# Kernel optimization log

Measured on AMD Instinct MI355X. Metric: run time of the kernel, lower is better.

The kernel has to match this reference:

```python
import jax, jax.numpy as jnp
import numpy as np

N = 50000      # n_nodes
E = 800000     # n_edges (before self loops)
DIN = 128      # in_channels
H = 4          # heads
C = 32         # out_channels per head  (H*C == DIN -> residual is Identity)
EPS = 1e-5
NEG_SLOPE = 0.2


def layer_norm(x, g, b):
    m = jnp.mean(x, axis=-1, keepdims=True)
    v = jnp.mean((x - m) ** 2, axis=-1, keepdims=True)
    return (x - m) * jax.lax.rsqrt(v + EPS) * g + b


def setup_inputs() -> dict:
    key = jax.random.key(0)
    ks = jax.random.split(key, 14)
    s = 1.0 / np.sqrt(DIN)
    return {
        "x": jax.random.normal(ks[0], (N, DIN), dtype=jnp.float32),
        "edge_index": jax.random.randint(ks[1], (2, E), 0, N, dtype=jnp.int64),
        "ln1_g": jnp.ones((DIN,), jnp.float32),
        "ln1_b": jnp.zeros((DIN,), jnp.float32),
        "W": jax.random.normal(ks[2], (DIN, H * C), jnp.float32) * s,
        "att_src": jax.random.normal(ks[3], (H, C), jnp.float32) * (1.0 / np.sqrt(C)),
        "att_dst": jax.random.normal(ks[4], (H, C), jnp.float32) * (1.0 / np.sqrt(C)),
        "gat_b": jnp.zeros((H * C,), jnp.float32),
        "ln2_g": jnp.ones((H * C,), jnp.float32),
        "ln2_b": jnp.zeros((H * C,), jnp.float32),
        "w1": jax.random.normal(ks[5], (H * C, 2 * H * C), jnp.float32) * (1.0 / np.sqrt(H * C)),
        "b1": jnp.zeros((2 * H * C,), jnp.float32),
        "w2": jax.random.normal(ks[6], (2 * H * C, H * C), jnp.float32) * (1.0 / np.sqrt(2 * H * C)),
        "b2": jnp.zeros((H * C,), jnp.float32),
    }


def gat_conv(h, src, dst, W, att_src, att_dst, gat_b, n):
    # linear projection per head: (n, H, C)
    xh = (h @ W).reshape(n, H, C)
    # per-node attention logits: (n, H)
    a_src = jnp.einsum("nhc,hc->nh", xh, att_src)
    a_dst = jnp.einsum("nhc,hc->nh", xh, att_dst)
    # edge scores + segment softmax over destination nodes
    alpha = jax.nn.leaky_relu(a_src[src] + a_dst[dst], NEG_SLOPE)  # (e, H)
    amax = jax.ops.segment_max(alpha, dst, num_segments=n)
    alpha = jnp.exp(alpha - amax[dst])
    denom = jax.ops.segment_sum(alpha, dst, num_segments=n)
    alpha = alpha / denom[dst]
    # weighted aggregation of source features
    msg = xh[src] * alpha[:, :, None]                                # (e, H, C)
    out = jax.ops.segment_sum(msg, dst, num_segments=n)              # (n, H, C)
    return out.reshape(n, H * C) + gat_b


def reference(x, edge_index, ln1_g, ln1_b, W, att_src, att_dst, gat_b,
              ln2_g, ln2_b, w1, b1, w2, b2):
    n = x.shape[0]
    # add self loops (PyG GATConv default add_self_loops=True)
    loops = jnp.arange(n, dtype=edge_index.dtype)
    src = jnp.concatenate([edge_index[0], loops])
    dst = jnp.concatenate([edge_index[1], loops])

    h = layer_norm(x, ln1_g, ln1_b)
    h = gat_conv(h, src, dst, W, att_src, att_dst, gat_b, n)
    h = h + x  # residual is Identity since in_channels == heads*out_channels
    hn = layer_norm(h, ln2_g, ln2_b)
    ffn = jax.nn.gelu(hn @ w1 + b1, approximate=False) @ w2 + b2
    return h + ffn
```

## Files before the change

### kernel.cpp

```cpp
#include <hip/hip_runtime.h>

#define DIN 128
#define HEADS 4
#define CPH 32
#define NEG_SLOPE 0.2f
#define LN_EPS 1e-5f
#define NPB 16
#define CS 4096
#define CE 512

typedef short bf16x8 __attribute__((ext_vector_type(8)));
typedef float f32x4 __attribute__((ext_vector_type(4)));
typedef float f32x2 __attribute__((ext_vector_type(2)));

__device__ __forceinline__ float wave_allsum(float v) {
#pragma unroll
    for (int off = 32; off > 0; off >>= 1) v += __shfl_down(v, off, 64);
    return __shfl(v, 0, 64);
}

__device__ __forceinline__ unsigned short f2bf(float f) {
    unsigned int b = __float_as_uint(f);
    b += 0x7FFFu + ((b >> 16) & 1u);
    return (unsigned short)(b >> 16);
}
__device__ __forceinline__ float bf2f(unsigned short u) {
    return __uint_as_float(((unsigned int)u) << 16);
}

#define ABST 136
#define HST  264
#define SRST 132

__global__ __launch_bounds__(256) void k_hist_pack(
    const int* __restrict__ ei, unsigned int* __restrict__ cnt, int E, int N, int Nper, int HB,
    const float* __restrict__ w1, const float* __restrict__ w2, const float* __restrict__ W,
    unsigned short* __restrict__ wp1, unsigned short* __restrict__ wp2,
    unsigned short* __restrict__ wpW)
{
    int bid = blockIdx.x;
    if (bid < HB) {
        int xcd = bid & 7, chunk = bid >> 3;
        int lo = xcd * Nper, hi = min(lo + Nper, N);
        int Et = E + N;
        int base = chunk * CS + threadIdx.x;
#pragma unroll
        for (int i = 0; i < CS / 256; ++i) {
            int e = base + i * 256;
            if (e >= Et) break;
            int d = (e < E) ? ei[E + e] : (e - E);
            if (d >= lo && d < hi) atomicAdd(&cnt[d], 1u);
        }
    } else {
        int idx = (bid - HB) * 256 + threadIdx.x;
        if (idx < 32768) {
            int j = idx & 7, lane = (idx >> 3) & 63, tk = idx >> 9;
            int ks = tk & 3, tile = tk >> 2;
            int k = ks * 32 + ((lane >> 4) << 3) + j;
            int n = tile * 16 + (lane & 15);
            wp1[idx] = f2bf(w1[k * 256 + n]);
        } else if (idx < 65536) {
            int i2 = idx - 32768;
            int j = i2 & 7, lane = (i2 >> 3) & 63, tk = i2 >> 9;
            int ks = tk & 7, tile = tk >> 3;
            int k = ks * 32 + ((lane >> 4) << 3) + j;
            int n = tile * 16 + (lane & 15);
            wp2[i2] = f2bf(w2[k * 128 + n]);
        } else {
            int i3 = idx - 65536;
            int j = i3 & 7, lane = (i3 >> 3) & 63, tk = i3 >> 9;
            int ks = tk & 3, tile = tk >> 2;
            int k = ks * 32 + ((lane >> 4) << 3) + j;
            int n = tile * 16 + (lane & 15);
            wpW[i3] = f2bf(W[k * 128 + n]);
        }
    }
}

__global__ __launch_bounds__(256) void k_partsum(
    const unsigned int* __restrict__ cnt, unsigned int* __restrict__ bsum, int N)
{
    __shared__ unsigned int sm[4];
    int t = threadIdx.x;
    int i = blockIdx.x * 256 + t;
    unsigned int v = (i < N) ? cnt[i] : 0u;
#pragma unroll
    for (int off = 32; off > 0; off >>= 1) v += (unsigned int)__shfl_down((int)v, off, 64);
    if ((t & 63) == 0) sm[t >> 6] = v;
    __syncthreads();
    if (t == 0) bsum[blockIdx.x] = sm[0] + sm[1] + sm[2] + sm[3];
}

__global__ __launch_bounds__(256) void k_scanb(
    const unsigned int* __restrict__ bsum, unsigned int* __restrict__ boff,
    unsigned int* __restrict__ row, int nb2, int N, int Et)
{
    __shared__ unsigned int sm[256];
    int t = threadIdx.x;
    unsigned int v = (t < nb2) ? bsum[t] : 0u;
    sm[t] = v;
    __syncthreads();
#pragma unroll
    for (int off = 1; off < 256; off <<= 1) {
        unsigned int a = (t >= off) ? sm[t - off] : 0u;
        __syncthreads();
        sm[t] += a;
        __syncthreads();
    }
    if (t < nb2) boff[t] = sm[t] - v;
    if (t == 0) row[N] = (unsigned int)Et;
}

__global__ __launch_bounds__(256) void k_scanw(
    const unsigned int* __restrict__ cnt, const unsigned int* __restrict__ boff,
    unsigned int* __restrict__ row, unsigned int* __restrict__ pos, int N)
{
    __shared__ unsigned int sm[256];
    int t = threadIdx.x;
    int i = blockIdx.x * 256 + t;
    unsigned int v = (i < N) ? cnt[i] : 0u;
    sm[t] = v;
    __syncthreads();
#pragma unroll
    for (int off = 1; off < 256; off <<= 1) {
        unsigned int a = (t >= off) ? sm[t - off] : 0u;
        __syncthreads();
        sm[t] += a;
        __syncthreads();
    }
    if (i < N) {
        unsigned int o = boff[blockIdx.x] + sm[t] - v;
        row[i] = o;
        pos[i] = o;
    }
}

__global__ __launch_bounds__(256) void k_scatter_proj(
    const int* __restrict__ ei, unsigned int* __restrict__ pos,
    int* __restrict__ srcs, int E, int N, int Nper, int SB,
    const float* __restrict__ x,
    const float* __restrict__ g1, const float* __restrict__ b1,
    const unsigned short* __restrict__ wpW,
    const float* __restrict__ att_src, const float* __restrict__ att_dst,
    unsigned short* __restrict__ xhb, float* __restrict__ a_src, float* __restrict__ a_dst)
{
    __shared__ __align__(16) unsigned short A_bf[NPB * ABST];
    __shared__ __align__(16) unsigned short sxh[NPB * ABST];
    int bid = blockIdx.x;
    int t = threadIdx.x;

    if (bid < SB) {
        int xcd = bid & 7, chunk = bid >> 3;
        int lo = xcd * Nper, hi = min(lo + Nper, N);
        int Et = E + N;
        int base = chunk * CS + t;
#pragma unroll
        for (int i = 0; i < CS / 256; ++i) {
            int e = base + i * 256;
            if (e >= Et) break;
            int d = (e < E) ? ei[E + e] : (e - E);
            if (d >= lo && d < hi) {
                int s = (e < E) ? ei[e] : d;
                unsigned int p = atomicAdd(&pos[d], 1u);
                srcs[p] = s;
            }
        }
        return;
    }

    int w = t >> 6, lane = t & 63;
    int quad = lane >> 4, l15 = lane & 15;
    int nbase = (bid - SB) * NPB;

#pragma unroll
    for (int i = 0; i < 4; ++i) {
        int nn = w * 4 + i;
        int n = nbase + nn;
        float x0 = 0.f, x1 = 0.f;
        if (n < N) { x0 = x[n * DIN + lane]; x1 = x[n * DIN + 64 + lane]; }
        float mean = wave_allsum(x0 + x1) * (1.0f / DIN);
        float d0 = x0 - mean, d1 = x1 - mean;
        float var = wave_allsum(d0 * d0 + d1 * d1) * (1.0f / DIN);
        float rstd = rsqrtf(var + LN_EPS);
        A_bf[nn * ABST + lane]      = f2bf(d0 * rstd * g1[lane]      + b1[lane]);
        A_bf[nn * ABST + 64 + lane] = f2bf(d1 * rstd * g1[64 + lane] + b1[64 + lane]);
    }
    __syncthreads();

    {
        int arow = l15 * ABST;
        bf16x8 afrag[4];
#pragma unroll
        for (int ks = 0; ks < 4; ++ks)
            afrag[ks] = *(const bf16x8*)&A_bf[arow + ks * 32 + quad * 8];
#pragma unroll
        for (int nt = 0; nt < 2; ++nt) {
            int tile = w * 2 + nt;
            f32x4 acc = {0.f, 0.f, 0.f, 0.f};
#pragma unroll
            for (int ks = 0; ks < 4; ++ks) {
                bf16x8 bfrag = *(const bf16x8*)&wpW[(((tile * 4 + ks) * 64 + lane) << 3)];
                acc = __builtin_amdgcn_mfma_f32_16x16x32_bf16(afrag[ks], bfrag, acc, 0, 0, 0);
            }
            int col = tile * 16 + l15;
#pragma unroll
            for (int reg = 0; reg < 4; ++reg)
                sxh[(quad * 4 + reg) * ABST + col] = f2bf(acc[reg]);
        }
    }
    __syncthreads();

    {
        int node = t >> 4, off = (t & 15) * 8;
        int n = nbase + node;
        if (n < N)
            *(uint4*)&xhb[(size_t)n * DIN + off] = *(const uint4*)&sxh[node * ABST + off];
    }

    {
        int node = w * 4 + (lane >> 4);
        int h = (lane >> 2) & 3, sub = lane & 3;
        float s1 = 0.f, s2 = 0.f;
#pragma unroll
        for (int i = 0; i < 8; ++i) {
            int c = h * CPH + sub * 8 + i;
            float v = bf2f(sxh[node * ABST + c]);
            s1 += v * att_src[c];
            s2 += v * att_dst[c];
        }
        s1 += __shfl_down(s1, 1, 64); s2 += __shfl_down(s2, 1, 64);
        s1 += __shfl_down(s1, 2, 64); s2 += __shfl_down(s2, 2, 64);
        int n = nbase + node;
        if (sub == 0 && n < N) {
            a_src[n * HEADS + h] = s1;
            a_dst[n * HEADS + h] = s2;
        }
    }
}

__global__ __launch_bounds__(256, 6) void k_agg_final(
    const unsigned int* __restrict__ row, const int* __restrict__ srcs,
    const float* __restrict__ a_src, const float* __restrict__ a_dst,
    const uint2* __restrict__ xhb2,
    const float* __restrict__ x,
    const float* __restrict__ gat_b,
    const float* __restrict__ g2, const float* __restrict__ b2g,
    const unsigned short* __restrict__ wp1, const float* __restrict__ bb1,
    const unsigned short* __restrict__ wp2, const float* __restrict__ bb2,
    float* __restrict__ out, int N)
{
    __shared__ __align__(16) unsigned char smem[21248];
    float*          shres  = (float*)smem;
    unsigned short* A_bf   = (unsigned short*)(smem + 8448);
    unsigned short* hid_bf = (unsigned short*)(smem + 12800);
    float*          s_p    = (float*)smem;
    int*            s_srcs = (int*)(smem + 8192);
    float*          s_adl  = (float*)(smem + 10240);
    int*            s_rowl = (int*)(smem + 10496);

    int t = threadIdx.x;
    int w = t >> 6, lane = t & 63;
    int quad = lane >> 4, l15 = lane & 15;
    int nbase = blockIdx.x * NPB;
    int half = lane >> 5;
    int li   = lane & 31;
    int h2   = li >> 3;

    f32x2 gbp, g2p, b2p;
    {
        const f32x2* gb2 = (const f32x2*)gat_b;
        const f32x2* gg2 = (const f32x2*)g2;
        const f32x2* bb2v = (const f32x2*)b2g;
        gbp = gb2[lane]; g2p = gg2[lane]; b2p = bb2v[lane];
    }

    if (t <= NPB) {
        int idx = nbase + t; if (idx > N) idx = N;
        s_rowl[t] = (int)row[idx];
    }
    if (t < 64) {
        int d = nbase + (t >> 2);
        s_adl[t] = (d < N) ? a_dst[d * HEADS + (t & 3)] : 0.f;
    }

    int nend = nbase + NPB; if (nend > N) nend = N;
    int estart = (int)row[nbase];
    int eend = (int)row[nend];

    int wr[5];
#pragma unroll
    for (int j = 0; j < 5; ++j) {
        int idx = nbase + w * 4 + j; if (idx > N) idx = N;
        wr[j] = (int)row[idx];
    }

    float o4[4][4];
    float den4[4];
#pragma unroll
    for (int i = 0; i < 4; ++i) {
        den4[i] = 0.f;
#pragma unroll
        for (int c = 0; c < 4; ++c) o4[i][c] = 0.f;
    }

    for (int cbase = estart; cbase < eend; cbase += CE) {
        int cnum = eend - cbase; if (cnum > CE) cnum = CE;
        int cend = cbase + cnum;
        __syncthreads();

        for (int e = t; e < cnum; e += 256) {
            int ge = cbase + e;
            int s = srcs[ge];
            s_srcs[e] = s;
            int node = 0;
#pragma unroll
            for (int k = 1; k <= NPB; ++k) node += (ge >= s_rowl[k]) ? 1 : 0;
            float4 as4 = *(const float4*)&a_src[s * 4];
            float4 ad4 = *(const float4*)&s_adl[node * 4];
            float4 pv;
            float a0 = as4.x + ad4.x; a0 = fmaxf(a0, NEG_SLOPE * a0); pv.x = __expf(a0);
            float a1 = as4.y + ad4.y; a1 = fmaxf(a1, NEG_SLOPE * a1); pv.y = __expf(a1);
            float a2 = as4.z + ad4.z; a2 = fmaxf(a2, NEG_SLOPE * a2); pv.z = __expf(a2);
            float a3 = as4.w + ad4.w; a3 = fmaxf(a3, NEG_SLOPE * a3); pv.w = __expf(a3);
            *(float4*)&s_p[e * 4] = pv;
        }
        __syncthreads();

#pragma unroll
        for (int i = 0; i < 4; ++i) {
            int lo = wr[i] > cbase ? wr[i] : cbase;
            int hi = wr[i + 1] < cend ? wr[i + 1] : cend;
            if (lo >= hi) continue;
            int e = lo - cbase;
            int eh = hi - cbase;
            float p0_ = o4[i][0], p1_ = o4[i][1], p2_ = o4[i][2], p3_ = o4[i][3];
            float den_ = den4[i];
            for (; e + 16 <= eh; e += 16) {
                uint2 uu[8]; float pp[8];
#pragma unroll
                for (int j = 0; j < 8; ++j) {
                    int s = s_srcs[e + 2 * j + half];
                    uu[j] = xhb2[s * 32 + li];
                }
#pragma unroll
                for (int j = 0; j < 8; ++j) pp[j] = s_p[((e + 2 * j + half) << 2) + h2];
#pragma unroll
                for (int j = 0; j < 8; ++j) {
                    den_ += pp[j];
                    p0_ += pp[j] * __uint_as_float(uu[j].x << 16);
                    p1_ += pp[j] * __uint_as_float(uu[j].x & 0xFFFF0000u);
                    p2_ += pp[j] * __uint_as_float(uu[j].y << 16);
                    p3_ += pp[j] * __uint_as_float(uu[j].y & 0xFFFF0000u);
                }
            }
            for (; e + 8 <= eh; e += 8) {
                uint2 uu[4]; float pp[4];
#pragma unroll
                for (int j = 0; j < 4; ++j) {
                    int s = s_srcs[e + 2 * j + half];
                    uu[j] = xhb2[s * 32 + li];
                }
#pragma unroll
                for (int j = 0; j < 4; ++j) pp[j] = s_p[((e + 2 * j + half) << 2) + h2];
#pragma unroll
                for (int j = 0; j < 4; ++j) {
                    den_ += pp[j];
                    p0_ += pp[j] * __uint_as_float(uu[j].x << 16);
                    p1_ += pp[j] * __uint_as_float(uu[j].x & 0xFFFF0000u);
                    p2_ += pp[j] * __uint_as_float(uu[j].y << 16);
                    p3_ += pp[j] * __uint_as_float(uu[j].y & 0xFFFF0000u);
                }
            }
            for (; e + 2 <= eh; e += 2) {
                int s = s_srcs[e + half];
                float p = s_p[((e + half) << 2) + h2];
                uint2 u = xhb2[s * 32 + li];
                den_ += p;
                p0_ += p * __uint_as_float(u.x << 16);
                p1_ += p * __uint_as_float(u.x & 0xFFFF0000u);
                p2_ += p * __uint_as_float(u.y << 16);
                p3_ += p * __uint_as_float(u.y & 0xFFFF0000u);
            }
            if (e < eh) {
                int s = s_srcs[e];
                float p = half ? 0.f : s_p[(e << 2) + h2];
                uint2 u = xhb2[s * 32 + li];
                den_ += p;
                p0_ += p * __uint_as_float(u.x << 16);
                p1_ += p * __uint_as_float(u.x & 0xFFFF0000u);
                p2_ += p * __uint_as_float(u.y << 16);
                p3_ += p * __uint_as_float(u.y & 0xFFFF0000u);
            }
            o4[i][0] = p0_; o4[i][1] = p1_; o4[i][2] = p2_; o4[i][3] = p3_;
            den4[i] = den_;
        }
    }
    __syncthreads();

#pragma unroll
    for (int i = 0; i < 4; ++i) {
        int nn = w * 4 + i;
        int d = nbase + nn;
        float c0 = o4[i][0] + __shfl_xor(o4[i][0], 32, 64);
        float c1 = o4[i][1] + __shfl_xor(o4[i][1], 32, 64);
        float c2 = o4[i][2] + __shfl_xor(o4[i][2], 32, 64);
        float c3 = o4[i][3] + __shfl_xor(o4[i][3], 32, 64);
        float dn = den4[i] + __shfl_xor(den4[i], 32, 64);
        int srcl = lane >> 1;
        float a0 = __shfl(c0, srcl, 64);
        float a1 = __shfl(c1, srcl, 64);
        float a2 = __shfl(c2, srcl, 64);
        float a3 = __shfl(c3, srcl, 64);
        float den_p = __shfl(dn, (lane >> 4) << 3, 64);
        float oo0 = (lane & 1) ? a2 : a0;
        float oo1 = (lane & 1) ? a3 : a1;

        float h0 = 0.f, h1 = 0.f;
        if (d < N) {
            float inv = 1.0f / den_p;
            f32x2 xv = ((const f32x2*)(x + (size_t)d * DIN))[lane];
            h0 = oo0 * inv + gbp.x + xv.x;
            h1 = oo1 * inv + gbp.y + xv.y;
        }
        float mean = wave_allsum(h0 + h1) * (1.0f / DIN);
        float d0 = h0 - mean, d1 = h1 - mean;
        float var = wave_allsum(d0 * d0 + d1 * d1) * (1.0f / DIN);
        float rstd = rsqrtf(var + LN_EPS);
        f32x2 hres; hres.x = h0; hres.y = h1;
        ((f32x2*)&shres[nn * SRST])[lane] = hres;
        unsigned int apk = (unsigned int)f2bf(d0 * rstd * g2p.x + b2p.x)
                         | ((unsigned int)f2bf(d1 * rstd * g2p.y + b2p.y) << 16);
        ((unsigned int*)&A_bf[nn * ABST])[lane] = apk;
    }
    __syncthreads();

    {
        int arow = l15 * ABST;
        bf16x8 afrag[4];
#pragma unroll
        for (int ks = 0; ks < 4; ++ks)
            afrag[ks] = *(const bf16x8*)&A_bf[arow + ks * 32 + quad * 8];
#pragma unroll
        for (int nt = 0; nt < 4; ++nt) {
            int tile = w * 4 + nt;
            f32x4 acc = {0.f, 0.f, 0.f, 0.f};
#pragma unroll
            for (int ks = 0; ks < 4; ++ks) {
                bf16x8 bfrag = *(const bf16x8*)&wp1[(((tile * 4 + ks) * 64 + lane) << 3)];
                acc = __builtin_amdgcn_mfma_f32_16x16x32_bf16(afrag[ks], bfrag, acc, 0, 0, 0);
            }
            int col = tile * 16 + l15;
            float bias = bb1[col];
#pragma unroll
            for (int reg = 0; reg < 4; ++reg) {
                int m_local = quad * 4 + reg;
                float a = acc[reg] + bias;
                float g = 0.5f * a * (1.0f + erff(a * 0.70710678118654752f));
                hid_bf[m_local * HST + col] = f2bf(g);
            }
        }
    }
    __syncthreads();

    {
        int arow = l15 * HST;
        bf16x8 afrag[8];
#pragma unroll
        for (int ks = 0; ks < 8; ++ks)
            afrag[ks] = *(const bf16x8*)&hid_bf[arow + ks * 32 + quad * 8];
#pragma unroll
        for (int nt = 0; nt < 2; ++nt) {
            int tile = w * 2 + nt;
            f32x4 acc = {0.f, 0.f, 0.f, 0.f};
#pragma unroll
            for (int ks = 0; ks < 8; ++ks) {
                bf16x8 bfrag = *(const bf16x8*)&wp2[(((tile * 8 + ks) * 64 + lane) << 3)];
                acc = __builtin_amdgcn_mfma_f32_16x16x32_bf16(afrag[ks], bfrag, acc, 0, 0, 0);
            }
            int j = tile * 16 + l15;
            float bias = bb2[j];
#pragma unroll
            for (int reg = 0; reg < 4; ++reg) {
                int m_local = quad * 4 + reg;
                int n = nbase + m_local;
                if (n < N)
                    out[(size_t)n * DIN + j] = shres[m_local * SRST + j] + acc[reg] + bias;
            }
        }
    }
}

extern "C" void kernel_launch(void* const* d_in, const int* in_sizes, int n_in,
                              void* d_out, int out_size, void* d_ws, size_t ws_size,
                              hipStream_t stream) {
    const float* x       = (const float*)d_in[0];
    const int*   ei      = (const int*)d_in[1];
    const float* ln1_g   = (const float*)d_in[2];
    const float* ln1_b   = (const float*)d_in[3];
    const float* W       = (const float*)d_in[4];
    const float* att_src = (const float*)d_in[5];
    const float* att_dst = (const float*)d_in[6];
    const float* gat_b   = (const float*)d_in[7];
    const float* ln2_g   = (const float*)d_in[8];
    const float* ln2_b   = (const float*)d_in[9];
    const float* w1      = (const float*)d_in[10];
    const float* b1      = (const float*)d_in[11];
    const float* w2      = (const float*)d_in[12];
    const float* b2      = (const float*)d_in[13];
    float* out = (float*)d_out;

    const int N = in_sizes[0] / DIN;
    const int E = in_sizes[1] / 2;
    const int Et = E + N;
    const int Nper = (N + 7) / 8;

    unsigned short* wp1 = (unsigned short*)d_ws;
    unsigned short* wp2 = wp1 + 32768;
    unsigned short* wpW = wp2 + 32768;
    unsigned short* xhb = wpW + 16384;
    float*        a_src = (float*)(xhb + (size_t)N * DIN);
    float*        a_dst = a_src + (size_t)N * HEADS;
    unsigned int* cnt  = (unsigned int*)(a_dst + (size_t)N * HEADS);
    unsigned int* row  = cnt + N;
    unsigned int* pos  = row + N + 1;
    unsigned int* bsum = pos + N;
    unsigned int* boff = bsum + 256;
    int*           srcs = (int*)(boff + 256);

    hipMemsetAsync(cnt, 0, (size_t)N * sizeof(unsigned int), stream);

    int nblocks = (N + NPB - 1) / NPB;
    int cblocks = (Et + CS - 1) / CS;
    int HB = cblocks * 8;
    int nb2 = (N + 255) / 256;

    k_hist_pack<<<HB + 320, 256, 0, stream>>>(ei, cnt, E, N, Nper, HB, w1, w2, W, wp1, wp2, wpW);

    k_partsum<<<nb2, 256, 0, stream>>>(cnt, bsum, N);
    k_scanb<<<1, 256, 0, stream>>>(bsum, boff, row, nb2, N, Et);
    k_scanw<<<nb2, 256, 0, stream>>>(cnt, boff, row, pos, N);

    k_scatter_proj<<<HB + nblocks, 256, 0, stream>>>(ei, pos, srcs, E, N, Nper, HB,
                                                     x, ln1_g, ln1_b, wpW, att_src, att_dst,
                                                     xhb, a_src, a_dst);

    k_agg_final<<<nblocks, 256, 0, stream>>>(row, srcs, a_src, a_dst, (const uint2*)xhb,
                                             x, gat_b, ln2_g, ln2_b, wp1, b1, wp2, b2, out, N);
}
```

Before: 255.7 us.

## Fuse three scan kernels into one decoupled scan and drop XCD-partitioned edge passes

Replaces the three-kernel prefix scan (partsum, block scan, write) with a single kernel. In it, the last block to finish computes the block offsets and publishes a flag that every other block spin-waits on. Histogram and scatter passes no longer replicate each edge chunk across 8 XCD-partitioned blocks that filter by destination range. Each edge is now read once and atomics go straight to global counters. This saves two launches and 8x redundant edge reads, at the cost of cross-XCD atomic contention and a spin-wait that assumes all 196 scan blocks are co-resident.

```diff
diff --git a/kernel.cpp b/kernel.cpp
--- a/kernel.cpp
+++ b/kernel.cpp
@@ -33,23 +33,20 @@
 #define SRST 132
 
 __global__ __launch_bounds__(256) void k_hist_pack(
-    const int* __restrict__ ei, unsigned int* __restrict__ cnt, int E, int N, int Nper, int HB,
+    const int* __restrict__ ei, unsigned int* __restrict__ cnt, int E, int Et, int HB,
     const float* __restrict__ w1, const float* __restrict__ w2, const float* __restrict__ W,
     unsigned short* __restrict__ wp1, unsigned short* __restrict__ wp2,
     unsigned short* __restrict__ wpW)
 {
     int bid = blockIdx.x;
     if (bid < HB) {
-        int xcd = bid & 7, chunk = bid >> 3;
-        int lo = xcd * Nper, hi = min(lo + Nper, N);
-        int Et = E + N;
-        int base = chunk * CS + threadIdx.x;
+        int base = bid * CS + threadIdx.x;
 #pragma unroll
         for (int i = 0; i < CS / 256; ++i) {
             int e = base + i * 256;
             if (e >= Et) break;
             int d = (e < E) ? ei[E + e] : (e - E);
-            if (d >= lo && d < hi) atomicAdd(&cnt[d], 1u);
+            atomicAdd(&cnt[d], 1u);
         }
     } else {
         int idx = (bid - HB) * 256 + threadIdx.x;
@@ -77,67 +74,80 @@
     }
 }
 
-__global__ __launch_bounds__(256) void k_partsum(
-    const unsigned int* __restrict__ cnt, unsigned int* __restrict__ bsum, int N)
+__global__ __launch_bounds__(256) void k_scan_fused(
+    const unsigned int* __restrict__ cnt,
+    unsigned int* __restrict__ done, unsigned int* __restrict__ flag,
+    unsigned int* __restrict__ bsum, unsigned int* __restrict__ boff,
+    unsigned int* __restrict__ row, unsigned int* __restrict__ pos, int N, int Et)
 {
-    __shared__ unsigned int sm[4];
+    __shared__ unsigned int ws[4];
+    __shared__ unsigned int s_tot;
+    __shared__ int s_last;
+    __shared__ unsigned int s_base;
     int t = threadIdx.x;
-    int i = blockIdx.x * 256 + t;
+    int lane = t & 63, wv = t >> 6;
+    int bid = blockIdx.x;
+    int nb = gridDim.x;
+    int i = bid * 256 + t;
+
     unsigned int v = (i < N) ? cnt[i] : 0u;
-#pragma unroll
-    for (int off = 32; off > 0; off >>= 1) v += (unsigned int)__shfl_down((int)v, off, 64);
-    if ((t & 63) == 0) sm[t >> 6] = v;
-    __syncthreads();
-    if (t == 0) bsum[blockIdx.x] = sm[0] + sm[1] + sm[2] + sm[3];
-}
-
-__global__ __launch_bounds__(256) void k_scanb(
-    const unsigned int* __restrict__ bsum, unsigned int* __restrict__ boff,
-    unsigned int* __restrict__ row, int nb2, int N, int Et)
-{
-    __shared__ unsigned int sm[256];
-    int t = threadIdx.x;
-    unsigned int v = (t < nb2) ? bsum[t] : 0u;
-    sm[t] = v;
-    __syncthreads();
-#pragma unroll
-    for (int off = 1; off < 256; off <<= 1) {
-        unsigned int a = (t >= off) ? sm[t - off] : 0u;
+    unsigned int s = v;
+#pragma unroll
+    for (int off = 1; off < 64; off <<= 1) {
+        unsigned int a = (unsigned int)__shfl_up((int)s, off, 64);
+        if (lane >= off) s += a;
+    }
+    if (lane == 63) ws[wv] = s;
+    __syncthreads();
+    if (t == 0) {
+        unsigned int a0 = ws[0], a1 = ws[1], a2 = ws[2], a3 = ws[3];
+        ws[0] = 0u; ws[1] = a0; ws[2] = a0 + a1; ws[3] = a0 + a1 + a2;
+        s_tot = a0 + a1 + a2 + a3;
+    }
+    __syncthreads();
+    unsigned int excl = ws[wv] + (s - v);
+
+    if (t == 0) {
+        __hip_atomic_store(&bsum[bid], s_tot, __ATOMIC_RELEASE, __HIP_MEMORY_SCOPE_AGENT);
+        unsigned int old = __hip_atomic_fetch_add(done, 1u, __ATOMIC_ACQ_REL, __HIP_MEMORY_SCOPE_AGENT);
+        s_last = (old == (unsigned int)(nb - 1)) ? 1 : 0;
+    }
+    __syncthreads();
+
+    if (s_last) {
+        unsigned int bv = (t < nb) ? __hip_atomic_load(&bsum[t], __ATOMIC_ACQUIRE, __HIP_MEMORY_SCOPE_AGENT) : 0u;
+        unsigned int sc = bv;
+#pragma unroll
+        for (int off = 1; off < 64; off <<= 1) {
+            unsigned int a = (unsigned int)__shfl_up((int)sc, off, 64);
+            if (lane >= off) sc += a;
+        }
+        if (lane == 63) ws[wv] = sc;
         __syncthreads();
-        sm[t] += a;
+        if (t == 0) {
+            unsigned int a0 = ws[0], a1 = ws[1], a2 = ws[2];
+            ws[0] = 0u; ws[1] = a0; ws[2] = a0 + a1; ws[3] = a0 + a1 + a2;
+        }
         __syncthreads();
-    }
-    if (t < nb2) boff[t] = sm[t] - v;
-    if (t == 0) row[N] = (unsigned int)Et;
-}
-
-__global__ __launch_bounds__(256) void k_scanw(
-    const unsigned int* __restrict__ cnt, const unsigned int* __restrict__ boff,
-    unsigned int* __restrict__ row, unsigned int* __restrict__ pos, int N)
-{
-    __shared__ unsigned int sm[256];
-    int t = threadIdx.x;
-    int i = blockIdx.x * 256 + t;
-    unsigned int v = (i < N) ? cnt[i] : 0u;
-    sm[t] = v;
-    __syncthreads();
-#pragma unroll
-    for (int off = 1; off < 256; off <<= 1) {
-        unsigned int a = (t >= off) ? sm[t - off] : 0u;
+        if (t < nb) boff[t] = ws[wv] + (sc - bv);
         __syncthreads();
-        sm[t] += a;
-        __syncthreads();
-    }
-    if (i < N) {
-        unsigned int o = boff[blockIdx.x] + sm[t] - v;
-        row[i] = o;
-        pos[i] = o;
-    }
+        if (t == 0) __hip_atomic_store(flag, 1u, __ATOMIC_RELEASE, __HIP_MEMORY_SCOPE_AGENT);
+    }
+
+    if (t == 0) {
+        while (__hip_atomic_load(flag, __ATOMIC_ACQUIRE, __HIP_MEMORY_SCOPE_AGENT) == 0u)
+            __builtin_amdgcn_s_sleep(8);
+        s_base = boff[bid];
+    }
+    __syncthreads();
+    unsigned int base = s_base;
+    if (i < N) { row[i] = base + excl; pos[i] = base + excl; }
+    if (bid == 0 && t == 0) row[N] = (unsigned int)Et;
 }
 
 __global__ __launch_bounds__(256) void k_scatter_proj(
     const int* __restrict__ ei, unsigned int* __restrict__ pos,
-    int* __restrict__ srcs, int E, int N, int Nper, int SB,
+    int* __restrict__ srcs, int E, int N, int Et, int SB,
     const float* __restrict__ x,
     const float* __restrict__ g1, const float* __restrict__ b1,
     const unsigned short* __restrict__ wpW,
@@ -150,20 +160,15 @@
     int t = threadIdx.x;
 
     if (bid < SB) {
-        int xcd = bid & 7, chunk = bid >> 3;
-        int lo = xcd * Nper, hi = min(lo + Nper, N);
-        int Et = E + N;
-        int base = chunk * CS + t;
+        int base = bid * CS + t;
 #pragma unroll
         for (int i = 0; i < CS / 256; ++i) {
             int e = base + i * 256;
             if (e >= Et) break;
             int d = (e < E) ? ei[E + e] : (e - E);
-            if (d >= lo && d < hi) {
-                int s = (e < E) ? ei[e] : d;
-                unsigned int p = atomicAdd(&pos[d], 1u);
-                srcs[p] = s;
-            }
+            int s = (e < E) ? ei[e] : d;
+            unsigned int p = atomicAdd(&pos[d], 1u);
+            srcs[p] = s;
         }
         return;
     }
@@ -512,7 +517,6 @@
     const int N = in_sizes[0] / DIN;
     const int E = in_sizes[1] / 2;
     const int Et = E + N;
-    const int Nper = (N + 7) / 8;
 
     unsigned short* wp1 = (unsigned short*)d_ws;
     unsigned short* wp2 = wp1 + 32768;
@@ -521,28 +525,27 @@
     float*        a_src = (float*)(xhb + (size_t)N * DIN);
     float*        a_dst = a_src + (size_t)N * HEADS;
     unsigned int* cnt  = (unsigned int*)(a_dst + (size_t)N * HEADS);
-    unsigned int* row  = cnt + N;
+    unsigned int* done = cnt + N;
+    unsigned int* flag = done + 1;
+    unsigned int* row  = flag + 1;
     unsigned int* pos  = row + N + 1;
     unsigned int* bsum = pos + N;
     unsigned int* boff = bsum + 256;
     int*           srcs = (int*)(boff + 256);
 
-    hipMemsetAsync(cnt, 0, (size_t)N * sizeof(unsigned int), stream);
+    hipMemsetAsync(cnt, 0, (size_t)(N + 2) * sizeof(unsigned int), stream);
 
     int nblocks = (N + NPB - 1) / NPB;
     int cblocks = (Et + CS - 1) / CS;
-    int HB = cblocks * 8;
     int nb2 = (N + 255) / 256;
 
-    k_hist_pack<<<HB + 320, 256, 0, stream>>>(ei, cnt, E, N, Nper, HB, w1, w2, W, wp1, wp2, wpW);
-
-    k_partsum<<<nb2, 256, 0, stream>>>(cnt, bsum, N);
-    k_scanb<<<1, 256, 0, stream>>>(bsum, boff, row, nb2, N, Et);
-    k_scanw<<<nb2, 256, 0, stream>>>(cnt, boff, row, pos, N);
-
-    k_scatter_proj<<<HB + nblocks, 256, 0, stream>>>(ei, pos, srcs, E, N, Nper, HB,
-                                                     x, ln1_g, ln1_b, wpW, att_src, att_dst,
-                                                     xhb, a_src, a_dst);
+    k_hist_pack<<<cblocks + 320, 256, 0, stream>>>(ei, cnt, E, Et, cblocks, w1, w2, W, wp1, wp2, wpW);
+
+    k_scan_fused<<<nb2, 256, 0, stream>>>(cnt, done, flag, bsum, boff, row, pos, N, Et);
+
+    k_scatter_proj<<<cblocks + nblocks, 256, 0, stream>>>(ei, pos, srcs, E, N, Et, cblocks,
+                                                          x, ln1_g, ln1_b, wpW, att_src, att_dst,
+                                                          xhb, a_src, a_dst);
 
     k_agg_final<<<nblocks, 256, 0, stream>>>(row, srcs, a_src, a_dst, (const uint2*)xhb,
                                              x, gat_b, ln2_g, ln2_b, wp1, b1, wp2, b2, out, N);
```

Result: slower. 262.3 us (+2.6%).
